# Performance work log

Measured on AMD Instinct MI355X. Metric: run time of the kernel, lower is better.

Reference implementation:

```python
import jax, jax.numpy as jnp
import numpy as np

GRID_LO = np.array([0.0, -3.2, -2.0], np.float32)
GRID_HI = np.array([6.4, 3.2, 2.0], np.float32)
VOXEL_SIZE = 0.4
P_MAX = 40   # voxel_point_max
V_NUM = 60   # voxel_num (top-k voxels by point count)
DIMS = np.round((GRID_HI - GRID_LO) / VOXEL_SIZE).astype(np.int32)  # [16, 16, 10]
NV = int(DIMS.prod())  # 2560 voxels
DYZ = int(DIMS[1] * DIMS[2])
KPT_ENC = np.array([
    [0,0,0,0,1,0],[0,0,0,1,0,0],[0,0,0,1,1,0],[0,0,1,0,0,0],[0,0,1,0,1,0],
    [0,0,1,1,0,0],[0,0,1,1,1,0],[0,1,0,0,0,0],[0,1,0,0,1,0],[0,1,0,1,0,0],
    [0,1,0,1,1,0],[0,1,1,0,0,0],[0,1,1,0,1,0],[0,1,1,1,0,0],[0,1,1,1,1,0],
    [1,0,0,0,0,0],[1,0,0,0,1,0]], np.float32)


def setup_inputs() -> dict:
    key = jax.random.key(0)
    k1, k2 = jax.random.split(key)
    B, N, n_kpt = 32, 400_000, 17
    lo = jnp.asarray(GRID_LO)
    hi = jnp.asarray(GRID_HI)
    pc = lo + (hi - lo) * jax.random.uniform(k1, (B, N, 3), jnp.float32)
    kpts = lo + (hi - lo) * jax.random.uniform(k2, (B, n_kpt, 3), jnp.float32)
    return {"pc": pc, "kpts": kpts}


def _voxelize_one(pc_b):
    # pc_b: (N, 3) -> pts (V, P, 3), vl_ids (V, 3)
    lo = jnp.asarray(GRID_LO)
    dims = jnp.asarray(DIMS)
    valid = jnp.any(pc_b != 0, axis=1)  # torch drops all-zero rows
    vl = ((pc_b - lo) / VOXEL_SIZE).astype(jnp.int32)  # trunc toward zero, like .long()
    inrange = jnp.all((vl >= 0) & (vl < dims), axis=1) & valid
    lin = vl[:, 0] * DYZ + vl[:, 1] * int(DIMS[2]) + vl[:, 2]
    lin = jnp.where(inrange, lin, NV)  # invalid points -> overflow bucket NV
    counts = jax.ops.segment_sum(jnp.ones_like(lin), lin, num_segments=NV + 1)
    order = jnp.argsort(lin)  # stable: preserves original point order within a voxel
    starts = jnp.cumsum(counts) - counts  # start offset of each voxel in sorted order
    top_cnt, top_vox = jax.lax.top_k(counts[:NV], V_NUM)  # descending by count
    cnt = jnp.maximum(top_cnt, 1)
    # slot p picks pt_indices[p % count] (torch repeat-tiling / first-P selection)
    pos = starts[top_vox][:, None] + (jnp.arange(P_MAX, dtype=jnp.int32)[None, :] % cnt[:, None])
    pts = pc_b[order[pos]]  # (V, P, 3)
    vx = top_vox // DYZ
    rem = top_vox % DYZ
    vox3 = jnp.stack([vx, rem // int(DIMS[2]), rem % int(DIMS[2])], axis=1).astype(jnp.float32)
    vl_ids = lo + vox3 * VOXEL_SIZE + VOXEL_SIZE / 2  # voxel centers
    return pts, vl_ids


def _kpt_cond_one(vl_ids, kpts_b):
    # vl_ids: (V, 3), kpts_b: (17, 3) -> (V, 6)
    kq = kpts_b[:, jnp.array([2, 0, 1])]
    d = jnp.linalg.norm(kq[:, None, :] - vl_ids[None, :, :], axis=-1)  # (17, V)
    md = jnp.min(d, axis=1)
    mi = jnp.argmin(d, axis=1)
    base = jnp.asarray(KPT_ENC)
    kc = jnp.zeros((V_NUM, 6), jnp.float32)
    for j in range(base.shape[0]):  # fixed small loop over 17 keypoints (sequential averaging)
        enc = base[j].at[5].set(md[j])
        row = kc[mi[j]]
        kc = kc.at[mi[j]].set(jnp.where(jnp.all(row == 0), enc, (row + enc) * 0.5))
    return kc


def reference(pc, kpts):
    pts, vl_ids = jax.vmap(_voxelize_one)(pc)
    kc = jax.vmap(_kpt_cond_one)(vl_ids, kpts)
    return pts, vl_ids, kc
```

## Files before the change

### kernel.cpp

```cpp
#include <hip/hip_runtime.h>
#include <hip/hip_bf16.h>

#define BN 32
#define NPTS 400000
#define NVOX 2560
#define GDYZ 160
#define GDZ 10
#define VN 60
#define PMAX 40
#define CAP 512

#define NCH_H 40
#define CHUNK_H (NPTS / NCH_H)
#define NCH_L 50
#define CHUNK_L (NPTS / NCH_L)

#define OFF_COUNTS 0
#define SZ_COUNTS (BN * NVOX * 4)
#define OFF_TICKETS (OFF_COUNTS + SZ_COUNTS)
#define SZ_TICKETS (BN * VN * 4)
#define OFF_TOPVOX (OFF_TICKETS + SZ_TICKETS)
#define OFF_TOPCNT (OFF_TOPVOX + BN * VN * 4)
#define OFF_SLOTMAP (OFF_TOPCNT + BN * VN * 4)
#define OFF_LISTS (OFF_SLOTMAP + BN * NVOX)
#define SZ_LISTS (BN * VN * CAP * 4)
#define OFF_VOX (OFF_LISTS + SZ_LISTS)
#define SZ_VOX (BN * NPTS * 2)
#define OFF_PART (OFF_VOX + SZ_VOX)
#define SZ_PART (BN * NCH_H * NVOX * 4)

#define OUT_PTS 0
#define OUT_VL (BN * VN * PMAX * 3)
#define OUT_KC (OUT_VL + BN * VN * 3)

__device__ __constant__ float KENC[17][5] = {
    {0,0,0,0,1},{0,0,0,1,0},{0,0,0,1,1},{0,0,1,0,0},{0,0,1,0,1},{0,0,1,1,0},
    {0,0,1,1,1},{0,1,0,0,0},{0,1,0,0,1},{0,1,0,1,0},{0,1,0,1,1},{0,1,1,0,0},
    {0,1,1,0,1},{0,1,1,1,0},{0,1,1,1,1},{1,0,0,0,0},{1,0,0,0,1}};

__device__ __forceinline__ int voxid(float x, float y, float z) {
    float ex = x;
    float ey = __fadd_rn(y, 3.2f);
    float ez = __fadd_rn(z, 2.0f);
    int vx = (int)(ex / 0.4f);
    int vy = (int)(ey / 0.4f);
    int vz = (int)(ez / 0.4f);
    bool valid = !(x == 0.0f && y == 0.0f && z == 0.0f);
    bool inr = (vx >= 0) & (vx < 16) & (vy >= 0) & (vy < 16) & (vz >= 0) & (vz < 10);
    return (valid && inr) ? (vx * GDYZ + vy * GDZ + vz) : 0xFFFF;
}

__global__ __launch_bounds__(256) void k_vox_hist(const float* __restrict__ pc,
        unsigned int* __restrict__ counts, unsigned short* __restrict__ vox,
        unsigned int* __restrict__ partials, int useVox, int usePart) {
    __shared__ unsigned int hist[NVOX];
    int b = blockIdx.x / NCH_H;
    int ch = blockIdx.x % NCH_H;
    for (int v = threadIdx.x; v < NVOX; v += 256) hist[v] = 0u;
    __syncthreads();
    const float4* p4 = (const float4*)(pc + (size_t)b * NPTS * 3);
    int start = ch * CHUNK_H, end = start + CHUNK_H;
    for (int g = start + threadIdx.x * 4; g < end; g += 256 * 4) {
        int f = (g * 3) >> 2;
        float4 q0 = p4[f], q1 = p4[f + 1], q2 = p4[f + 2];
        float xs[4] = {q0.x, q0.w, q1.z, q2.y};
        float ys[4] = {q0.y, q1.x, q1.w, q2.z};
        float zs[4] = {q0.z, q1.y, q2.x, q2.w};
        unsigned short ids[4];
#pragma unroll
        for (int k = 0; k < 4; ++k) {
            int id = voxid(xs[k], ys[k], zs[k]);
            ids[k] = (unsigned short)id;
            if (id < NVOX) atomicAdd(&hist[id], 1u);
        }
        if (useVox)
            *(ushort4*)(&vox[(size_t)b * NPTS + g]) =
                make_ushort4(ids[0], ids[1], ids[2], ids[3]);
    }
    __syncthreads();
    if (usePart) {
        unsigned int* dst = partials + ((size_t)b * NCH_H + ch) * NVOX;
        for (int v = threadIdx.x; v < NVOX; v += 256) dst[v] = hist[v];
    } else {
        for (int v = threadIdx.x; v < NVOX; v += 256) {
            unsigned int c = hist[v];
            if (c) atomicAdd(&counts[b * NVOX + v], c);
        }
    }
}

__global__ __launch_bounds__(256) void k_reduce_counts(
        const uint4* __restrict__ partials4, uint4* __restrict__ counts4) {
    int t = blockIdx.x * 256 + threadIdx.x;
    if (t >= BN * NVOX / 4) return;
    int b = t / (NVOX / 4), q = t % (NVOX / 4);
    const uint4* src = partials4 + (size_t)b * NCH_H * (NVOX / 4) + q;
    uint4 s = make_uint4(0u, 0u, 0u, 0u);
#pragma unroll 8
    for (int c = 0; c < NCH_H; ++c) {
        uint4 w = src[(size_t)c * (NVOX / 4)];
        s.x += w.x; s.y += w.y; s.z += w.z; s.w += w.w;
    }
    counts4[t] = s;
}

__global__ __launch_bounds__(64) void k_topk(const unsigned int* __restrict__ counts,
        int* __restrict__ topvox, int* __restrict__ topcnt,
        unsigned char* __restrict__ slotmap, unsigned int* __restrict__ tickets,
        float* __restrict__ out) {
    __shared__ unsigned int keys[NVOX];
    __shared__ int svox[VN];
    int b = blockIdx.x;
    int tid = threadIdx.x;
    unsigned int mloc = 0u;
    for (int v = tid; v < NVOX; v += 64) {
        unsigned int k = (counts[b * NVOX + v] << 12) | (unsigned int)(4095 - v);
        keys[v] = k;
        if (k > mloc) mloc = k;
    }
    {
        unsigned int* d32 = (unsigned int*)(slotmap + b * NVOX);
        for (int w = tid; w < NVOX / 4; w += 64) d32[w] = 0xFFFFFFFFu;
    }
    if (tid < VN) tickets[b * VN + tid] = 0u;
    __syncthreads();
    for (int r = 0; r < VN; ++r) {
        unsigned int m = mloc;
#pragma unroll
        for (int o = 32; o > 0; o >>= 1) {
            unsigned int t2 = __shfl_xor(m, o, 64);
            if (t2 > m) m = t2;
        }
        if (mloc == m) {
            int v = 4095 - (int)(m & 4095u);
            topvox[b * VN + r] = v;
            topcnt[b * VN + r] = (int)(m >> 12);
            slotmap[b * NVOX + v] = (unsigned char)r;
            svox[r] = v;
            keys[v] = 0u;
            mloc = 0u;
            for (int vv = tid; vv < NVOX; vv += 64) {
                unsigned int k = keys[vv];
                if (k > mloc) mloc = k;
            }
        }
    }
    __syncthreads();
    if (tid < VN) {
        int v = svox[tid];
        int vx = v / GDYZ, rem = v % GDYZ, vy = rem / GDZ, vz = rem % GDZ;
        float c0 = __fadd_rn(__fmul_rn((float)vx, 0.4f), 0.2f);
        float c1 = __fadd_rn(__fadd_rn(-3.2f, __fmul_rn((float)vy, 0.4f)), 0.2f);
        float c2 = __fadd_rn(__fadd_rn(-2.0f, __fmul_rn((float)vz, 0.4f)), 0.2f);
        float* vl = out + OUT_VL + (b * VN + tid) * 3;
        vl[0] = c0; vl[1] = c1; vl[2] = c2;
    }
}

__global__ __launch_bounds__(256) void k_build_lists(const float* __restrict__ pc,
        const unsigned short* __restrict__ vox, int useVox,
        const unsigned char* __restrict__ slotmap,
        unsigned int* __restrict__ tickets, unsigned int* __restrict__ lists) {
    __shared__ unsigned char smap[NVOX];
    int b = blockIdx.x / NCH_L;
    int ch = blockIdx.x % NCH_L;
    {
        const unsigned int* s32 = (const unsigned int*)(slotmap + b * NVOX);
        unsigned int* d32 = (unsigned int*)smap;
        for (int v = threadIdx.x; v < NVOX / 4; v += 256) d32[v] = s32[v];
    }
    __syncthreads();
    int start = ch * CHUNK_L, end = start + CHUNK_L;
    if (useVox) {
        const unsigned short* vb = vox + (size_t)b * NPTS;
        for (int i = start + threadIdx.x * 8; i < end; i += 256 * 8) {
            uint4 w = *(const uint4*)(vb + i);
            unsigned int ids[8] = {w.x & 0xFFFFu, w.x >> 16, w.y & 0xFFFFu, w.y >> 16,
                                   w.z & 0xFFFFu, w.z >> 16, w.w & 0xFFFFu, w.w >> 16};
#pragma unroll
            for (int k = 0; k < 8; ++k) {
                if (ids[k] < NVOX) {
                    unsigned char s = smap[ids[k]];
                    if (s != 0xFF) {
                        unsigned int t = atomicAdd(&tickets[b * VN + s], 1u);
                        if (t < CAP) lists[(size_t)(b * VN + s) * CAP + t] =
                                         (unsigned int)(i + k);
                    }
                }
            }
        }
    } else {
        const float* pb = pc + (size_t)b * NPTS * 3;
        for (int i = start + threadIdx.x; i < end; i += 256) {
            int id = voxid(pb[i * 3], pb[i * 3 + 1], pb[i * 3 + 2]);
            if (id < NVOX) {
                unsigned char s = smap[id];
                if (s != 0xFF) {
                    unsigned int t = atomicAdd(&tickets[b * VN + s], 1u);
                    if (t < CAP) lists[(size_t)(b * VN + s) * CAP + t] = (unsigned int)i;
                }
            }
        }
    }
}

__global__ __launch_bounds__(64) void k_select_kc(const float* __restrict__ pc,
        const float* __restrict__ kpts,
        const int* __restrict__ topvox, const int* __restrict__ topcnt,
        const unsigned int* __restrict__ lists, float* __restrict__ out) {
    __shared__ unsigned int sorted[PMAX];
    __shared__ float vl_s[VN * 3];
    __shared__ float kc_s[VN * 6];
    __shared__ float md_s[17];
    __shared__ int mi_s[17];
    int bs = blockIdx.x;
    int lane = threadIdx.x;

    if (bs >= BN * VN) {
        int b = bs - BN * VN;
        const float* vl = out + OUT_VL + b * VN * 3;
        for (int i = lane; i < VN * 3; i += 64) vl_s[i] = vl[i];
        for (int i = lane; i < VN * 6; i += 64) kc_s[i] = 0.0f;
        __syncthreads();
        if (lane < 17) {
            const float* kp = kpts + b * 17 * 3 + lane * 3;
            float a0 = kp[2], a1 = kp[0], a2 = kp[1];
            float best = 1e30f;
            int bi = 0;
            for (int i = 0; i < VN; ++i) {
                float d0 = __fsub_rn(a0, vl_s[i * 3 + 0]);
                float d1 = __fsub_rn(a1, vl_s[i * 3 + 1]);
                float d2 = __fsub_rn(a2, vl_s[i * 3 + 2]);
                float sq = __fadd_rn(__fadd_rn(__fmul_rn(d0, d0), __fmul_rn(d1, d1)),
                                     __fmul_rn(d2, d2));
                float d = __fsqrt_rn(sq);
                if (d < best) { best = d; bi = i; }
            }
            md_s[lane] = best;
            mi_s[lane] = bi;
        }
        __syncthreads();
        if (lane == 0) {
            for (int j = 0; j < 17; ++j) {
                float e[6] = {KENC[j][0], KENC[j][1], KENC[j][2], KENC[j][3],
                              KENC[j][4], md_s[j]};
                float* row = kc_s + mi_s[j] * 6;
                bool z = true;
                for (int q = 0; q < 6; ++q) z = z && (row[q] == 0.0f);
                for (int q = 0; q < 6; ++q)
                    row[q] = z ? e[q] : __fmul_rn(__fadd_rn(row[q], e[q]), 0.5f);
            }
        }
        __syncthreads();
        float* kc = out + OUT_KC + b * VN * 6;
        for (int i = lane; i < VN * 6; i += 64) kc[i] = kc_s[i];
        return;
    }

    int b = bs / VN;
    int cnt = topcnt[bs];
    float* po = out + OUT_PTS + (size_t)bs * PMAX * 3;
    if (cnt == 0) {
        for (int t = lane; t < PMAX * 3; t += 64) po[t] = 0.0f;
        return;
    }
    int K = cnt < PMAX ? cnt : PMAX;
    if (cnt <= CAP) {
        const unsigned int* L = lists + (size_t)bs * CAP;
        unsigned int vals[CAP / 64];
#pragma unroll
        for (int q = 0; q < CAP / 64; ++q) {
            int e = lane + q * 64;
            vals[q] = (e < cnt) ? L[e] : 0xFFFFFFFFu;
        }
        unsigned int lastp = 0u;
        for (int r = 0; r < K; ++r) {
            unsigned int m = 0xFFFFFFFFu;
#pragma unroll
            for (int q = 0; q < CAP / 64; ++q) {
                unsigned int v = vals[q];
                if (v >= lastp && v < m) m = v;
            }
#pragma unroll
            for (int o = 32; o > 0; o >>= 1) {
                unsigned int t = __shfl_xor(m, o, 64);
                m = (t < m) ? t : m;
            }
            if (lane == 0) sorted[r] = m;
            lastp = m + 1u;
        }
    } else {
        const float* pb = pc + (size_t)b * NPTS * 3;
        int v = topvox[bs];
        int k = 0;
        for (int base = 0; base < NPTS && k < PMAX; base += 64) {
            int i = base + lane;
            int id = voxid(pb[i * 3], pb[i * 3 + 1], pb[i * 3 + 2]);
            unsigned long long mask = __ballot(id == v);
            if (id == v) {
                int rk = k + (int)__popcll(mask & ((1ull << lane) - 1ull));
                if (rk < PMAX) sorted[rk] = (unsigned int)i;
            }
            k += (int)__popcll(mask);
        }
    }
    __syncthreads();
    for (int t = lane; t < PMAX * 3; t += 64) {
        int j = t / 3, kk = t % 3;
        int jj = (cnt >= PMAX) ? j : (j % cnt);
        unsigned int idx = sorted[jj];
        po[t] = pc[((size_t)b * NPTS + idx) * 3 + kk];
    }
}

extern "C" void kernel_launch(void* const* d_in, const int* in_sizes, int n_in,
                              void* d_out, int out_size, void* d_ws, size_t ws_size,
                              hipStream_t stream) {
    const float* pc = (const float*)d_in[0];
    const float* kpts = (const float*)d_in[1];
    float* out = (float*)d_out;
    char* ws = (char*)d_ws;

    unsigned int* counts = (unsigned int*)(ws + OFF_COUNTS);
    unsigned int* tickets = (unsigned int*)(ws + OFF_TICKETS);
    int* topvox = (int*)(ws + OFF_TOPVOX);
    int* topcnt = (int*)(ws + OFF_TOPCNT);
    unsigned char* slotmap = (unsigned char*)(ws + OFF_SLOTMAP);
    unsigned int* lists = (unsigned int*)(ws + OFF_LISTS);
    unsigned short* vox = (unsigned short*)(ws + OFF_VOX);
    unsigned int* partials = (unsigned int*)(ws + OFF_PART);
    int useVox = (ws_size >= (size_t)OFF_PART) ? 1 : 0;
    int usePart = (ws_size >= (size_t)(OFF_PART + SZ_PART)) ? 1 : 0;

    if (!usePart)
        hipMemsetAsync(ws + OFF_COUNTS, 0, SZ_COUNTS, stream);

    hipLaunchKernelGGL(k_vox_hist, dim3(BN * NCH_H), dim3(256), 0, stream,
                       pc, counts, vox, partials, useVox, usePart);
    if (usePart)
        hipLaunchKernelGGL(k_reduce_counts, dim3((BN * NVOX / 4 + 255) / 256),
                           dim3(256), 0, stream,
                           (const uint4*)partials, (uint4*)counts);
    hipLaunchKernelGGL(k_topk, dim3(BN), dim3(64), 0, stream,
                       counts, topvox, topcnt, slotmap, tickets, out);
    hipLaunchKernelGGL(k_build_lists, dim3(BN * NCH_L), dim3(256), 0, stream,
                       pc, vox, useVox, slotmap, tickets, lists);
    hipLaunchKernelGGL(k_select_kc, dim3(BN * VN + BN), dim3(64), 0, stream,
                       pc, kpts, topvox, topcnt, lists, out);
}
```

Before: 148.6 us.

## Fuse partial-count reduction into top-k and use radix-style threshold selection

Drops the separate reduce kernel and has the top-k block sum the per-chunk histogram partials directly, with the histogram chunk count cut from 40 to 16 so fewer partials need summing. The 60-round sequential argmax is replaced by a binary search for the 60th-largest key, followed by candidate compaction and rank-by-counting. This saves a launch and the serial top-k rounds. In exchange, the histogram kernel launches far fewer blocks (512) over longer chunks, which may reduce its parallelism.

```diff
diff --git a/kernel.cpp b/kernel.cpp
--- a/kernel.cpp
+++ b/kernel.cpp
@@ -10,7 +10,7 @@
 #define PMAX 40
 #define CAP 512
 
-#define NCH_H 40
+#define NCH_H 16
 #define CHUNK_H (NPTS / NCH_H)
 #define NCH_L 50
 #define CHUNK_L (NPTS / NCH_L)
@@ -89,71 +89,74 @@
     }
 }
 
-__global__ __launch_bounds__(256) void k_reduce_counts(
-        const uint4* __restrict__ partials4, uint4* __restrict__ counts4) {
-    int t = blockIdx.x * 256 + threadIdx.x;
-    if (t >= BN * NVOX / 4) return;
-    int b = t / (NVOX / 4), q = t % (NVOX / 4);
-    const uint4* src = partials4 + (size_t)b * NCH_H * (NVOX / 4) + q;
-    uint4 s = make_uint4(0u, 0u, 0u, 0u);
-#pragma unroll 8
-    for (int c = 0; c < NCH_H; ++c) {
-        uint4 w = src[(size_t)c * (NVOX / 4)];
-        s.x += w.x; s.y += w.y; s.z += w.z; s.w += w.w;
-    }
-    counts4[t] = s;
-}
-
-__global__ __launch_bounds__(64) void k_topk(const unsigned int* __restrict__ counts,
+__global__ __launch_bounds__(256) void k_topk(
+        const unsigned int* __restrict__ partials,
+        const unsigned int* __restrict__ counts, int usePart,
         int* __restrict__ topvox, int* __restrict__ topcnt,
         unsigned char* __restrict__ slotmap, unsigned int* __restrict__ tickets,
         float* __restrict__ out) {
     __shared__ unsigned int keys[NVOX];
-    __shared__ int svox[VN];
+    __shared__ unsigned int cand[VN];
+    __shared__ unsigned int ncand;
     int b = blockIdx.x;
     int tid = threadIdx.x;
-    unsigned int mloc = 0u;
-    for (int v = tid; v < NVOX; v += 64) {
-        unsigned int k = (counts[b * NVOX + v] << 12) | (unsigned int)(4095 - v);
-        keys[v] = k;
-        if (k > mloc) mloc = k;
+    if (usePart) {
+#pragma unroll
+        for (int k = 0; k < NVOX / 256; ++k) {
+            int v = tid + 256 * k;
+            const unsigned int* src = partials + (size_t)b * NCH_H * NVOX + v;
+            unsigned int s = 0;
+#pragma unroll
+            for (int c = 0; c < NCH_H; ++c) s += src[(size_t)c * NVOX];
+            keys[v] = (s << 12) | (unsigned int)(4095 - v);
+        }
+    } else {
+        for (int v = tid; v < NVOX; v += 256)
+            keys[v] = (counts[b * NVOX + v] << 12) | (unsigned int)(4095 - v);
     }
     {
         unsigned int* d32 = (unsigned int*)(slotmap + b * NVOX);
-        for (int w = tid; w < NVOX / 4; w += 64) d32[w] = 0xFFFFFFFFu;
+        for (int w = tid; w < NVOX / 4; w += 256) d32[w] = 0xFFFFFFFFu;
     }
     if (tid < VN) tickets[b * VN + tid] = 0u;
-    __syncthreads();
-    for (int r = 0; r < VN; ++r) {
-        unsigned int m = mloc;
-#pragma unroll
-        for (int o = 32; o > 0; o >>= 1) {
-            unsigned int t2 = __shfl_xor(m, o, 64);
-            if (t2 > m) m = t2;
-        }
-        if (mloc == m) {
-            int v = 4095 - (int)(m & 4095u);
+    if (tid == 0) ncand = 0u;
+    __syncthreads();
+    if (tid < 64) {
+        unsigned int kr[NVOX / 64];
+#pragma unroll
+        for (int j = 0; j < NVOX / 64; ++j) kr[j] = keys[tid + 64 * j];
+        unsigned int lo = 1u, hi = 0x80000000u;
+        while (lo < hi) {
+            unsigned int mid = lo + ((hi - lo + 1u) >> 1);
+            int c = 0;
+#pragma unroll
+            for (int j = 0; j < NVOX / 64; ++j) c += (kr[j] >= mid) ? 1 : 0;
+#pragma unroll
+            for (int o = 32; o > 0; o >>= 1) c += __shfl_xor(c, o, 64);
+            if (c >= VN) lo = mid; else hi = mid - 1u;
+        }
+#pragma unroll
+        for (int j = 0; j < NVOX / 64; ++j) {
+            if (kr[j] >= lo) {
+                unsigned int p = atomicAdd(&ncand, 1u);
+                cand[p] = kr[j];
+            }
+        }
+        if (tid < VN) {
+            unsigned int ki = cand[tid];
+            int r = 0;
+            for (int j = 0; j < VN; ++j) r += (cand[j] > ki) ? 1 : 0;
+            int v = 4095 - (int)(ki & 4095u);
             topvox[b * VN + r] = v;
-            topcnt[b * VN + r] = (int)(m >> 12);
+            topcnt[b * VN + r] = (int)(ki >> 12);
             slotmap[b * NVOX + v] = (unsigned char)r;
-            svox[r] = v;
-            keys[v] = 0u;
-            mloc = 0u;
-            for (int vv = tid; vv < NVOX; vv += 64) {
-                unsigned int k = keys[vv];
-                if (k > mloc) mloc = k;
-            }
-        }
-    }
-    __syncthreads();
-    if (tid < VN) {
-        int v = svox[tid];
-        int vx = v / GDYZ, rem = v % GDYZ, vy = rem / GDZ, vz = rem % GDZ;
-        float c0 = __fadd_rn(__fmul_rn((float)vx, 0.4f), 0.2f);
-        float c1 = __fadd_rn(__fadd_rn(-3.2f, __fmul_rn((float)vy, 0.4f)), 0.2f);
-        float c2 = __fadd_rn(__fadd_rn(-2.0f, __fmul_rn((float)vz, 0.4f)), 0.2f);
-        float* vl = out + OUT_VL + (b * VN + tid) * 3;
-        vl[0] = c0; vl[1] = c1; vl[2] = c2;
+            int vx = v / GDYZ, rem = v % GDYZ, vy = rem / GDZ, vz = rem % GDZ;
+            float c0 = __fadd_rn(__fmul_rn((float)vx, 0.4f), 0.2f);
+            float c1 = __fadd_rn(__fadd_rn(-3.2f, __fmul_rn((float)vy, 0.4f)), 0.2f);
+            float c2 = __fadd_rn(__fadd_rn(-2.0f, __fmul_rn((float)vz, 0.4f)), 0.2f);
+            float* vl = out + OUT_VL + (b * VN + r) * 3;
+            vl[0] = c0; vl[1] = c1; vl[2] = c2;
+        }
     }
 }
 
@@ -337,12 +340,9 @@
 
     hipLaunchKernelGGL(k_vox_hist, dim3(BN * NCH_H), dim3(256), 0, stream,
                        pc, counts, vox, partials, useVox, usePart);
-    if (usePart)
-        hipLaunchKernelGGL(k_reduce_counts, dim3((BN * NVOX / 4 + 255) / 256),
-                           dim3(256), 0, stream,
-                           (const uint4*)partials, (uint4*)counts);
-    hipLaunchKernelGGL(k_topk, dim3(BN), dim3(64), 0, stream,
-                       counts, topvox, topcnt, slotmap, tickets, out);
+    hipLaunchKernelGGL(k_topk, dim3(BN), dim3(256), 0, stream,
+                       partials, counts, usePart, topvox, topcnt, slotmap,
+                       tickets, out);
     hipLaunchKernelGGL(k_build_lists, dim3(BN * NCH_L), dim3(256), 0, stream,
                        pc, vox, useVox, slotmap, tickets, lists);
     hipLaunchKernelGGL(k_select_kc, dim3(BN * VN + BN), dim3(64), 0, stream,
```

Measured after the change: 130.3 us (median of 2 runs). 1.14x faster.
